# Performance work log

Hardware: AMD Instinct MI355X
Metric: run time of the kernel (lower is better)

Reference implementation:

```python
import jax, jax.numpy as jnp
import numpy as np

B, N, H, DH = 2, 512, 12, 64
DIM, DPAIR, DCOND = 768, 128, 512
INNER = 4 * DIM  # expansion_factor * dim


def _ln(x, eps=1e-5):
    m = jnp.mean(x, -1, keepdims=True)
    v = jnp.mean((x - m) ** 2, -1, keepdims=True)
    return (x - m) * jax.lax.rsqrt(v + eps)


def _rope(t):
    # t: [b,h,n,d]; standard rotary over head dim
    d = t.shape[-1]
    pos = jnp.arange(t.shape[2], dtype=t.dtype)
    inv = 1.0 / (10000.0 ** (jnp.arange(0, d, 2, dtype=t.dtype) / d))
    ang = pos[:, None] * inv[None, :]  # [n, d/2]
    cos, sin = jnp.cos(ang), jnp.sin(ang)
    t1, t2 = t[..., 0::2], t[..., 1::2]
    return jnp.stack([t1 * cos - t2 * sin, t1 * sin + t2 * cos], -1).reshape(t.shape)


def _adaln(x, cond, mask, gw, gb, bw):
    cn = _ln(cond)
    return (_ln(x) * jax.nn.sigmoid(cn @ gw + gb) + cn @ bw) * mask[..., None]


def _scale_out(x, cond, mask, w, b):
    # adaLN-zero style output scaling
    return x * jax.nn.sigmoid(_ln(cond) @ w + b) * mask[..., None]


def _windowed_attn(q, k, v, bias, pair_mask, n_queries, n_keys):
    # q/k/v: [b,h,n,d]; bias: [b,h,n,n]; pair_mask: [b,n,n]
    b, h, n, d = q.shape
    nw = n // n_queries
    centers = jnp.arange(nw) * n_queries + n_queries // 2
    idx = centers[:, None] - n_keys // 2 + jnp.arange(n_keys)[None, :]  # [nw,nk]
    valid = (idx >= 0) & (idx < n)
    idxc = jnp.clip(idx, 0, n - 1)
    qw = q.reshape(b, h, nw, n_queries, d)
    kw = k[:, :, idxc]  # [b,h,nw,nk,d]
    vw = v[:, :, idxc]
    ib = jnp.broadcast_to(idxc[None, None, :, None, :], (b, h, nw, n_queries, n_keys))
    bias_w = jnp.take_along_axis(bias.reshape(b, h, nw, n_queries, n), ib, axis=-1)
    pm = jnp.take_along_axis(
        pair_mask.reshape(b, nw, n_queries, n),
        jnp.broadcast_to(idxc[None, :, None, :], (b, nw, n_queries, n_keys)), axis=-1)
    scores = jnp.einsum('bhwqd,bhwkd->bhwqk', qw, kw) / jnp.sqrt(jnp.asarray(d, q.dtype)) + bias_w
    ok = (pm[:, None] > 0) & valid[None, None, :, None, :]
    attn = jax.nn.softmax(jnp.where(ok, scores, -1e9), axis=-1)
    out = jnp.einsum('bhwqk,bhwkd->bhwqd', attn, vw)
    return out.reshape(b, h, n, d)


def setup_inputs() -> dict:
    key = jax.random.key(0)
    ks = iter(jax.random.split(key, 48))
    nrm = lambda shape: jax.random.normal(next(ks), shape, jnp.float32) * 0.02
    return dict(
        x=jax.random.normal(next(ks), (B, N, DIM), jnp.float32),
        pair_rep=jax.random.normal(next(ks), (B, N, N, DPAIR), jnp.float32),
        cond=jax.random.normal(next(ks), (B, N, DCOND), jnp.float32),
        mask=jnp.ones((B, N), jnp.float32),
        pair_mask=jnp.ones((B, N, N), jnp.float32),
        adaln1_gw=nrm((DCOND, DIM)), adaln1_gb=jnp.zeros((DIM,), jnp.float32), adaln1_bw=nrm((DCOND, DIM)),
        wq=nrm((DIM, H * DH)), bq=jnp.zeros((H * DH,), jnp.float32),
        wk=nrm((DIM, H * DH)), bk=jnp.zeros((H * DH,), jnp.float32),
        wv=nrm((DIM, H * DH)), bv=jnp.zeros((H * DH,), jnp.float32),
        wg=nrm((DIM, H * DH)), bg=jnp.zeros((H * DH,), jnp.float32),
        wb_pair=nrm((DPAIR, H)),
        wo=nrm((H * DH, DIM)), bo=jnp.zeros((DIM,), jnp.float32),
        scale1_w=nrm((DCOND, DIM)), scale1_b=jnp.full((DIM,), -2.0, jnp.float32),
        adaln2_gw=nrm((DCOND, DIM)), adaln2_gb=jnp.zeros((DIM,), jnp.float32), adaln2_bw=nrm((DCOND, DIM)),
        tr_win=nrm((DIM, 2 * INNER)), tr_wout=nrm((INNER, DIM)),
        scale2_w=nrm((DCOND, DIM)), scale2_b=jnp.full((DIM,), -2.0, jnp.float32),
        n_queries=32, n_keys=128,
    )


def reference(x, pair_rep, cond, mask, pair_mask,
              adaln1_gw, adaln1_gb, adaln1_bw,
              wq, bq, wk, bk, wv, bv, wg, bg, wb_pair, wo, bo,
              scale1_w, scale1_b,
              adaln2_gw, adaln2_gb, adaln2_bw,
              tr_win, tr_wout,
              scale2_w, scale2_b,
              n_queries, n_keys):
    b, n, _ = x.shape
    x = x * mask[..., None]

    # --- MHA (adaLN -> pair-biased rotary windowed attention -> adaLN-zero scale) ---
    xa = _adaln(x, cond, mask, adaln1_gw, adaln1_gb, adaln1_bw)
    q = (xa @ wq + bq).reshape(b, n, H, DH).transpose(0, 2, 1, 3)
    k = (xa @ wk + bk).reshape(b, n, H, DH).transpose(0, 2, 1, 3)
    v = (xa @ wv + bv).reshape(b, n, H, DH).transpose(0, 2, 1, 3)
    q, k = _ln(q), _ln(k)      # qk layernorm
    q, k = _rope(q), _rope(k)  # rotary
    bias = jnp.einsum('bijp,ph->bhij', _ln(pair_rep), wb_pair)
    o = _windowed_attn(q, k, v, bias, pair_mask, n_queries, n_keys)
    o = o.transpose(0, 2, 1, 3).reshape(b, n, H * DH)
    attn_out = (o * jax.nn.sigmoid(xa @ wg + bg)) @ wo + bo
    attn_out = _scale_out(attn_out, cond, mask, scale1_w, scale1_b) * mask[..., None]
    x = (attn_out + x) * mask[..., None]  # residual_mha

    # --- Transition (adaLN -> SwiGLU -> adaLN-zero scale) ---
    xt = _adaln(x, cond, mask, adaln2_gw, adaln2_gb, adaln2_bw)
    a, g = jnp.split(xt @ tr_win, 2, axis=-1)
    tr = ((a * jax.nn.silu(g)) @ tr_wout) * mask[..., None]
    tr = _scale_out(tr, cond, mask, scale2_w, scale2_b) * mask[..., None]
    x = (tr + x) * mask[..., None]  # residual_transition
    return x * mask[..., None]
```

## Files before the change

### kernel.cpp

```cpp
#include <hip/hip_runtime.h>
#include <hip/hip_bf16.h>
#include <math.h>
#include <stdint.h>

#define Bc   2
#define Nc   512
#define Hc   12
#define DHc  64
#define DIMc 768
#define DPAIRc 128
#define DCONDc 512
#define INNERc 3072
#define NQc  32
#define NKc  128
#define NWc  (Nc / NQc)

typedef __attribute__((ext_vector_type(8))) short short8;
typedef __attribute__((ext_vector_type(4))) float floatx4;

__device__ inline float wave_sum(float v) {
#pragma unroll
  for (int off = 32; off > 0; off >>= 1) v += __shfl_xor(v, off, 64);
  return v;
}
__device__ inline float wave_max(float v) {
#pragma unroll
  for (int off = 32; off > 0; off >>= 1) v = fmaxf(v, __shfl_xor(v, off, 64));
  return v;
}
__device__ inline float block_sum(float v, float* red) {
  v = wave_sum(v);
  int wv = threadIdx.x >> 6, lane = threadIdx.x & 63;
  __syncthreads();
  if (lane == 0) red[wv] = v;
  __syncthreads();
  return red[0] + red[1] + red[2] + red[3];
}
__device__ inline float sigmoidf(float x) { return 1.0f / (1.0f + expf(-x)); }

__device__ __forceinline__ void gload16(const void* g, void* l) {
  __builtin_amdgcn_global_load_lds(
      reinterpret_cast<__attribute__((address_space(1))) const void*>(
          reinterpret_cast<uintptr_t>(g)),
      reinterpret_cast<__attribute__((address_space(3))) void*>(
          static_cast<uint32_t>(reinterpret_cast<uintptr_t>(l))),
      16, 0, 0);
}

__global__ __launch_bounds__(256) void ln_rows_bf16_k(const float* __restrict__ in,
                                                      __hip_bfloat16* __restrict__ out, int C) {
  __shared__ float red[4];
  int row = blockIdx.x;
  const float* x = in + (size_t)row * C;
  float s = 0.f;
  for (int c = threadIdx.x; c < C; c += 256) s += x[c];
  float mean = block_sum(s, red) / C;
  float vs = 0.f;
  for (int c = threadIdx.x; c < C; c += 256) { float d = x[c] - mean; vs += d * d; }
  float var = block_sum(vs, red) / C;
  float r = rsqrtf(var + 1e-5f);
  for (int c = threadIdx.x; c < C; c += 256)
    out[(size_t)row * C + c] = __float2bfloat16((x[c] - mean) * r);
}

struct TP6 { const float* s0; const float* s1; const float* s2;
             const float* s3; const float* s4; const float* s5; };
__global__ __launch_bounds__(256) void transpose_cast_batch_k(TP6 p,
    __hip_bfloat16* __restrict__ dstBase, int K, int N) {
  __shared__ float tile[32][33];
  const float* srcs[6] = {p.s0, p.s1, p.s2, p.s3, p.s4, p.s5};
  const float* src = srcs[blockIdx.z];
  __hip_bfloat16* dst = dstBase + (size_t)blockIdx.z * K * N;
  int k0 = blockIdx.y * 32, n0 = blockIdx.x * 32;
  int t = threadIdx.x;
  int r = t >> 5, c = t & 31;
#pragma unroll
  for (int i = 0; i < 4; ++i) tile[r + i * 8][c] = src[(size_t)(k0 + r + i * 8) * N + n0 + c];
  __syncthreads();
#pragma unroll
  for (int i = 0; i < 4; ++i)
    dst[(size_t)(n0 + r + i * 8) * K + k0 + c] = __float2bfloat16(tile[c][r + i * 8]);
}

__global__ __launch_bounds__(256) void concat_bias_k(
    const float* __restrict__ a1_gb, const float* __restrict__ s1_b,
    const float* __restrict__ a2_gb, const float* __restrict__ s2_b,
    const float* __restrict__ bq, const float* __restrict__ bk,
    const float* __restrict__ bv, const float* __restrict__ bg,
    const float* __restrict__ wb_pair,
    float* __restrict__ cb6, float* __restrict__ bqkvg,
    __hip_bfloat16* __restrict__ wbT, float* __restrict__ colsum) {
  int i = blockIdx.x * 256 + threadIdx.x;
  if (i < 6 * DIMc) {
    int seg = i / DIMc, o = i - seg * DIMc;
    float v = 0.f;
    if (seg == 0) v = a1_gb[o];
    else if (seg == 2) v = s1_b[o];
    else if (seg == 3) v = a2_gb[o];
    else if (seg == 5) v = s2_b[o];
    cb6[i] = v;
  }
  if (i < 4 * DIMc) {
    int seg = i / DIMc, o = i - seg * DIMc;
    bqkvg[i] = (seg == 0) ? bq[o] : (seg == 1) ? bk[o] : (seg == 2) ? bv[o] : bg[o];
  }
  if (i < 16 * DPAIRc) {
    int h = i >> 7, c = i & 127;
    wbT[i] = (h < Hc) ? __float2bfloat16(wb_pair[c * Hc + h]) : __float2bfloat16(0.f);
  }
  if (blockIdx.x == 0 && threadIdx.x < 16) {
    int h = threadIdx.x;
    float s = 0.f;
    if (h < Hc)
      for (int c = 0; c < DPAIRc; ++c)
        s += __bfloat162float(__float2bfloat16(wb_pair[c * Hc + h]));
    colsum[h] = s;
  }
}

template <int WNT>
__global__ __launch_bounds__(256) void gemm_bf16_k(
    const __hip_bfloat16* __restrict__ A, const __hip_bfloat16* __restrict__ Bt,
    float* __restrict__ C, int M, int N, int K,
    const float* __restrict__ bias,
    const float* __restrict__ ss, int ssst,
    const float* __restrict__ resid, const float* __restrict__ maskp, int mode) {
  constexpr int TN = 32 * WNT;
  __shared__ __align__(16) __hip_bfloat16 As[128 * 32];
  __shared__ __align__(16) __hip_bfloat16 Bs[TN * 32];
  int tid = threadIdx.x;
  int lane = tid & 63, wv = tid >> 6;
  int l16 = lane & 15, quad = lane >> 4;
  int m0 = blockIdx.y * 128, n0 = blockIdx.x * TN;
  int wm0 = (wv >> 1) * 64, wn0 = (wv & 1) * (16 * WNT);

  int srow = tid >> 2;
  int skc = (tid & 3) * 8;
  const __hip_bfloat16* Ab  = A  + (size_t)(m0 + srow) * K + skc;
  const __hip_bfloat16* Ab2 = Ab + (size_t)64 * K;
  const __hip_bfloat16* Bb  = Bt + (size_t)(n0 + srow) * K + skc;
  const __hip_bfloat16* Bb2 = Bb + (size_t)64 * K;
  __hip_bfloat16* AsW = As + wv * 512;
  __hip_bfloat16* BsW = Bs + wv * 512;

  floatx4 acc[4][WNT];
#pragma unroll
  for (int mi = 0; mi < 4; ++mi)
#pragma unroll
    for (int nj = 0; nj < WNT; ++nj) acc[mi][nj] = (floatx4){0.f, 0.f, 0.f, 0.f};

  for (int k0 = 0; k0 < K; k0 += 32) {
    gload16(Ab + k0, AsW);
    gload16(Ab2 + k0, AsW + 2048);
    if (WNT == 4) {
      gload16(Bb + k0, BsW);
      gload16(Bb2 + k0, BsW + 2048);
    } else {
      if (wv < 2) gload16(Bb + k0, BsW);
    }
    __syncthreads();
    short8 a[4], b[WNT];
#pragma unroll
    for (int mi = 0; mi < 4; ++mi)
      a[mi] = *(const short8*)(const void*)&As[(wm0 + mi * 16 + l16) * 32 + quad * 8];
#pragma unroll
    for (int nj = 0; nj < WNT; ++nj)
      b[nj] = *(const short8*)(const void*)&Bs[(wn0 + nj * 16 + l16) * 32 + quad * 8];
#pragma unroll
    for (int mi = 0; mi < 4; ++mi)
#pragma unroll
      for (int nj = 0; nj < WNT; ++nj)
        acc[mi][nj] = __builtin_amdgcn_mfma_f32_16x16x32_bf16(a[mi], b[nj], acc[mi][nj], 0, 0, 0);
    __syncthreads();
  }

#pragma unroll
  for (int mi = 0; mi < 4; ++mi) {
#pragma unroll
    for (int nj = 0; nj < WNT; ++nj) {
      int ncol = n0 + wn0 + nj * 16 + l16;
      float bb = bias ? bias[ncol] : 0.f;
#pragma unroll
      for (int r = 0; r < 4; ++r) {
        int m = m0 + wm0 + mi * 16 + quad * 4 + r;
        float v = acc[mi][nj][r] + bb;
        if (mode == 1) {
          float mk = maskp[m];
          v *= sigmoidf(ss[(size_t)m * ssst + ncol]) * mk * mk;
          v = (v + resid[(size_t)m * N + ncol]) * mk;
        } else if (mode == 2) {
          float mk = maskp[m];
          v = v * mk * sigmoidf(ss[(size_t)m * ssst + ncol]) * mk * mk;
          v = (v + resid[(size_t)m * N + ncol]) * mk * mk;
        }
        C[(size_t)m * N + ncol] = v;
      }
    }
  }
}

__global__ __launch_bounds__(256) void adaln_apply_k(
    const float* __restrict__ xin, const float* __restrict__ maskp,
    const float* __restrict__ graw, const float* __restrict__ braw, int ssst,
    __hip_bfloat16* __restrict__ xa, float* __restrict__ xm) {
  __shared__ float red[4];
  int row = blockIdx.x;
  float mk = maskp[row];
  const float* xr = xin + (size_t)row * DIMc;
  float vals[3];
  float s = 0.f;
#pragma unroll
  for (int it = 0; it < 3; ++it) {
    int c = threadIdx.x + it * 256;
    float v = xr[c] * mk;
    vals[it] = v;
    s += v;
  }
  float mean = block_sum(s, red) * (1.0f / DIMc);
  float vs = 0.f;
#pragma unroll
  for (int it = 0; it < 3; ++it) { float d = vals[it] - mean; vs += d * d; }
  float var = block_sum(vs, red) * (1.0f / DIMc);
  float r = rsqrtf(var + 1e-5f);
#pragma unroll
  for (int it = 0; it < 3; ++it) {
    int c = threadIdx.x + it * 256;
    size_t sidx = (size_t)row * ssst + c;
    if (xm) xm[(size_t)row * DIMc + c] = vals[it];
    float o = ((vals[it] - mean) * r * sigmoidf(graw[sidx]) + braw[sidx]) * mk;
    xa[(size_t)row * DIMc + c] = __float2bfloat16(o);
  }
}

__global__ __launch_bounds__(256) void lnrope_k(float* __restrict__ qkvg) {
  float* q = qkvg + blockIdx.y * DIMc;
  int rowid = blockIdx.x * 4 + (threadIdx.x >> 6);
  int lane = threadIdx.x & 63;
  int bn = rowid / Hc;
  int h = rowid - bn * Hc;
  int n = bn & (Nc - 1);
  size_t base = (size_t)bn * (4 * DIMc) + h * DHc;
  float v = q[base + lane];
  float mean = wave_sum(v) * (1.0f / 64.0f);
  float d = v - mean;
  float var = wave_sum(d * d) * (1.0f / 64.0f);
  float vn = d * rsqrtf(var + 1e-5f);
  int i = lane >> 1;
  float inv = exp2f(-(float)i * 0.415241011861f);
  float ang = (float)n * inv;
  float c = cosf(ang), s = sinf(ang);
  float partner = __shfl_xor(vn, 1, 64);
  float out = (lane & 1) ? (partner * s + vn * c) : (vn * c - partner * s);
  q[base + lane] = out;
}

__global__ __launch_bounds__(256) void pair_bias_mfma_k(
    const float* __restrict__ pr, const __hip_bfloat16* __restrict__ wbT,
    const float* __restrict__ colsum, float* __restrict__ biasw) {
  constexpr int LDR = 136;
  __shared__ __hip_bfloat16 rows[128 * LDR];
  __shared__ float meanS[128];
  __shared__ float rstdS[128];
  int bi = blockIdx.x;
  int i = bi & (Nc - 1), b = bi >> 9;
  int w = i >> 5, qi = i & 31;
  int j0 = w * NQc - 48;
  int t = threadIdx.x;
  int sub = t >> 5;
  int c4 = t & 31;
  const float* prb = pr + (size_t)bi * (Nc * DPAIRc);
#pragma unroll
  for (int step = 0; step < 16; ++step) {
    int row = step * 8 + sub;
    int jc = min(max(j0 + row, 0), Nc - 1);
    float4 v = *(const float4*)(prb + (size_t)jc * DPAIRc + c4 * 4);
    union { __hip_bfloat16 h[4]; uint2 u; } pk;
    pk.h[0] = __float2bfloat16(v.x); pk.h[1] = __float2bfloat16(v.y);
    pk.h[2] = __float2bfloat16(v.z); pk.h[3] = __float2bfloat16(v.w);
    *(uint2*)(void*)&rows[row * LDR + c4 * 4] = pk.u;
    float s = v.x + v.y + v.z + v.w;
    float s2 = v.x * v.x + v.y * v.y + v.z * v.z + v.w * v.w;
#pragma unroll
    for (int off = 16; off > 0; off >>= 1) {
      s += __shfl_xor(s, off, 64);
      s2 += __shfl_xor(s2, off, 64);
    }
    if (c4 == 0) {
      float mean = s * (1.0f / 128.0f);
      float var = s2 * (1.0f / 128.0f) - mean * mean;
      meanS[row] = mean;
      rstdS[row] = rsqrtf(var + 1e-5f);
    }
  }
  __syncthreads();
  int lane = t & 63, wv = t >> 6;
  int l16 = lane & 15, quad = lane >> 4;
  short8 bfrag[4];
#pragma unroll
  for (int ks = 0; ks < 4; ++ks)
    bfrag[ks] = *(const short8*)(const void*)&wbT[l16 * 128 + ks * 32 + quad * 8];
  float cs = colsum[l16];
#pragma unroll
  for (int mt = 0; mt < 2; ++mt) {
    int mtile = wv * 2 + mt;
    floatx4 acc = (floatx4){0.f, 0.f, 0.f, 0.f};
#pragma unroll
    for (int ks = 0; ks < 4; ++ks) {
      short8 a = *(const short8*)(const void*)&rows[(mtile * 16 + l16) * LDR + ks * 32 + quad * 8];
      acc = __builtin_amdgcn_mfma_f32_16x16x32_bf16(a, bfrag[ks], acc, 0, 0, 0);
    }
    if (l16 < Hc) {
      int m0r = mtile * 16 + quad * 4;
      float4 ov;
      float* po = &ov.x;
#pragma unroll
      for (int r = 0; r < 4; ++r) {
        int m = m0r + r;
        po[r] = rstdS[m] * (acc[r] - meanS[m] * cs);
      }
      *(float4*)&biasw[((((size_t)(b * Hc + l16)) * NWc + w) * NQc + qi) * NKc + m0r] = ov;
    }
  }
}

__global__ __launch_bounds__(256) void wattn_k(
    const float* __restrict__ qkvg, const float* __restrict__ biasw,
    const float* __restrict__ pair_mask, __hip_bfloat16* __restrict__ o) {
  constexpr int LQ = 72;
  constexpr int LV = 136;
  constexpr int LS = 132;
  constexpr int LP = 136;
  __shared__ __hip_bfloat16 qs[32 * LQ];
  __shared__ __hip_bfloat16 ks[128 * LQ];
  __shared__ __hip_bfloat16 vT[64 * LV];
  __shared__ float sc[32 * LS];
  __shared__ __hip_bfloat16 scP[32 * LP];
  const int QS = 4 * DIMc;
  int blk = blockIdx.x;
  int w = blk & (NWc - 1);
  int bh = blk >> 4;
  int h = bh % Hc;
  int b = bh / Hc;
  int t = threadIdx.x;
  int j0 = w * NQc - 48;
  for (int e = t; e < 512; e += 256) {
    int qrow = e >> 4, c4 = e & 15;
    float4 v = *(const float4*)&qkvg[(size_t)(b * Nc + w * NQc + qrow) * QS + h * DHc + c4 * 4];
    union { __hip_bfloat16 hh[4]; uint2 u; } pk;
    pk.hh[0] = __float2bfloat16(v.x); pk.hh[1] = __float2bfloat16(v.y);
    pk.hh[2] = __float2bfloat16(v.z); pk.hh[3] = __float2bfloat16(v.w);
    *(uint2*)(void*)&qs[qrow * LQ + c4 * 4] = pk.u;
  }
  for (int e = t; e < 2048; e += 256) {
    int kk = e >> 4, c4 = e & 15;
    int jc = min(max(j0 + kk, 0), Nc - 1);
    size_t src = (size_t)(b * Nc + jc) * QS + h * DHc + c4 * 4;
    float4 kv = *(const float4*)&qkvg[src + DIMc];
    float4 vv = *(const float4*)&qkvg[src + 2 * DIMc];
    union { __hip_bfloat16 hh[4]; uint2 u; } pk;
    pk.hh[0] = __float2bfloat16(kv.x); pk.hh[1] = __float2bfloat16(kv.y);
    pk.hh[2] = __float2bfloat16(kv.z); pk.hh[3] = __float2bfloat16(kv.w);
    *(uint2*)(void*)&ks[kk * LQ + c4 * 4] = pk.u;
    vT[(c4 * 4 + 0) * LV + kk] = __float2bfloat16(vv.x);
    vT[(c4 * 4 + 1) * LV + kk] = __float2bfloat16(vv.y);
    vT[(c4 * 4 + 2) * LV + kk] = __float2bfloat16(vv.z);
    vT[(c4 * 4 + 3) * LV + kk] = __float2bfloat16(vv.w);
  }
  for (int e = t; e < 4096; e += 256) {
    int qrow = e >> 7, key = e & 127;
    int j = j0 + key;
    bool valid = (j >= 0) && (j < Nc);
    int jc = min(max(j, 0), Nc - 1);
    float pm = pair_mask[((size_t)(b * Nc + w * NQc + qrow)) * Nc + jc];
    bool ok = valid && (pm > 0.f);
    sc[qrow * LS + key] = ok ? biasw[((size_t)blk * 32 + qrow) * 128 + key] : -1e30f;
  }
  __syncthreads();
  int lane = t & 63, wv = t >> 6;
  int l16 = lane & 15, quad = lane >> 4;
  {
    short8 bfr[2][2];
#pragma unroll
    for (int nt = 0; nt < 2; ++nt)
#pragma unroll
      for (int k2 = 0; k2 < 2; ++k2)
        bfr[nt][k2] = *(const short8*)(const void*)&ks[(wv * 32 + nt * 16 + l16) * LQ + k2 * 32 + quad * 8];
#pragma unroll
    for (int mi = 0; mi < 2; ++mi) {
      short8 afr[2];
#pragma unroll
      for (int k2 = 0; k2 < 2; ++k2)
        afr[k2] = *(const short8*)(const void*)&qs[(mi * 16 + l16) * LQ + k2 * 32 + quad * 8];
#pragma unroll
      for (int nt = 0; nt < 2; ++nt) {
        floatx4 acc = (floatx4){0.f, 0.f, 0.f, 0.f};
        acc = __builtin_amdgcn_mfma_f32_16x16x32_bf16(afr[0], bfr[nt][0], acc, 0, 0, 0);
        acc = __builtin_amdgcn_mfma_f32_16x16x32_bf16(afr[1], bfr[nt][1], acc, 0, 0, 0);
        int key = wv * 32 + nt * 16 + l16;
#pragma unroll
        for (int r = 0; r < 4; ++r) {
          int m = mi * 16 + quad * 4 + r;
          float sv = sc[m * LS + key];
          if (sv > -1e29f) sc[m * LS + key] = sv + acc[r] * 0.125f;
        }
      }
    }
  }
  __syncthreads();
#pragma unroll
  for (int rr = 0; rr < 8; ++rr) {
    int qq = wv * 8 + rr;
    float v0 = sc[qq * LS + lane], v1 = sc[qq * LS + 64 + lane];
    float mx = wave_max(fmaxf(v0, v1));
    float e0 = expf(v0 - mx), e1 = expf(v1 - mx);
    float inv = 1.0f / wave_sum(e0 + e1);
    scP[qq * LP + lane] = __float2bfloat16(e0 * inv);
    scP[qq * LP + 64 + lane] = __float2bfloat16(e1 * inv);
  }
  __syncthreads();
  {
    short8 vb[4];
#pragma unroll
    for (int k4 = 0; k4 < 4; ++k4)
      vb[k4] = *(const short8*)(const void*)&vT[(wv * 16 + l16) * LV + k4 * 32 + quad * 8];
#pragma unroll
    for (int mi = 0; mi < 2; ++mi) {
      floatx4 acc = (floatx4){0.f, 0.f, 0.f, 0.f};
#pragma unroll
      for (int k4 = 0; k4 < 4; ++k4) {
        short8 pa = *(const short8*)(const void*)&scP[(mi * 16 + l16) * LP + k4 * 32 + quad * 8];
        acc = __builtin_amdgcn_mfma_f32_16x16x32_bf16(pa, vb[k4], acc, 0, 0, 0);
      }
      int d = wv * 16 + l16;
#pragma unroll
      for (int r = 0; r < 4; ++r) {
        int m = mi * 16 + quad * 4 + r;
        size_t mrow = (size_t)(b * Nc + w * NQc + m);
        float g = qkvg[mrow * QS + 3 * DIMc + h * DHc + d];
        o[mrow * DIMc + h * DHc + d] = __float2bfloat16(acc[r] * sigmoidf(g));
      }
    }
  }
}

__global__ __launch_bounds__(256) void silu_gate_k(const float* __restrict__ h,
                                                   __hip_bfloat16* __restrict__ act, int total) {
  int i = blockIdx.x * 256 + threadIdx.x;
  if (i < total) {
    int m = i / INNERc, j = i - m * INNERc;
    float a = h[(size_t)m * (2 * INNERc) + j];
    float g = h[(size_t)m * (2 * INNERc) + INNERc + j];
    act[i] = __float2bfloat16(a * g * sigmoidf(g));
  }
}

extern "C" void kernel_launch(void* const* d_in, const int* in_sizes, int n_in,
                              void* d_out, int out_size, void* d_ws, size_t ws_size,
                              hipStream_t stream) {
  const float* x        = (const float*)d_in[0];
  const float* pair_rep = (const float*)d_in[1];
  const float* cond     = (const float*)d_in[2];
  const float* mask     = (const float*)d_in[3];
  const float* pair_mask= (const float*)d_in[4];
  const float* a1_gw    = (const float*)d_in[5];
  const float* a1_gb    = (const float*)d_in[6];
  const float* a1_bw    = (const float*)d_in[7];
  const float* wq       = (const float*)d_in[8];
  const float* bq       = (const float*)d_in[9];
  const float* wk       = (const float*)d_in[10];
  const float* bk       = (const float*)d_in[11];
  const float* wv       = (const float*)d_in[12];
  const float* bv       = (const float*)d_in[13];
  const float* wg       = (const float*)d_in[14];
  const float* bg       = (const float*)d_in[15];
  const float* wb_pair  = (const float*)d_in[16];
  const float* wo       = (const float*)d_in[17];
  const float* bo       = (const float*)d_in[18];
  const float* s1_w     = (const float*)d_in[19];
  const float* s1_b     = (const float*)d_in[20];
  const float* a2_gw    = (const float*)d_in[21];
  const float* a2_gb    = (const float*)d_in[22];
  const float* a2_bw    = (const float*)d_in[23];
  const float* tr_win   = (const float*)d_in[24];
  const float* tr_wout  = (const float*)d_in[25];
  const float* s2_w     = (const float*)d_in[26];
  const float* s2_b     = (const float*)d_in[27];
  float* out = (float*)d_out;

  const int M = Bc * Nc;
  char* wsb = (char*)d_ws;
  size_t off = 0;
  auto alloc = [&](size_t bytes) { void* p = wsb + off; off += (bytes + 255) & ~(size_t)255; return p; };

  __hip_bfloat16* cnb     = (__hip_bfloat16*)alloc((size_t)M * DCONDc * 2);
  __hip_bfloat16* Wc6t    = (__hip_bfloat16*)alloc((size_t)6 * DIMc * DCONDc * 2);
  __hip_bfloat16* Wqkvg5t = (__hip_bfloat16*)alloc((size_t)5 * DIMc * DIMc * 2);
  __hip_bfloat16* twint   = (__hip_bfloat16*)alloc((size_t)2 * INNERc * DIMc * 2);
  __hip_bfloat16* twoutt  = (__hip_bfloat16*)alloc((size_t)DIMc * INNERc * 2);
  float* cb6    = (float*)alloc((size_t)6 * DIMc * 4);
  float* bqkvg  = (float*)alloc((size_t)4 * DIMc * 4);
  __hip_bfloat16* wbT = (__hip_bfloat16*)alloc((size_t)16 * DPAIRc * 2);
  float* colsum = (float*)alloc(16 * 4);
  float* proj_c = (float*)alloc((size_t)M * 6 * DIMc * 4);
  float* xm     = (float*)alloc((size_t)M * DIMc * 4);
  __hip_bfloat16* xa = (__hip_bfloat16*)alloc((size_t)M * DIMc * 2);
  float* qkvg   = (float*)alloc((size_t)M * 4 * DIMc * 4);
  float* biasw  = (float*)alloc((size_t)Bc * Hc * NWc * NQc * NKc * 4);
  __hip_bfloat16* obg = (__hip_bfloat16*)alloc((size_t)M * DIMc * 2);
  float* x2     = (float*)alloc((size_t)M * DIMc * 4);
  __hip_bfloat16* xt = (__hip_bfloat16*)alloc((size_t)M * DIMc * 2);
  float* hb     = (float*)alloc((size_t)M * 2 * INNERc * 4);
  __hip_bfloat16* actb = (__hip_bfloat16*)alloc((size_t)M * INNERc * 2);
  __hip_bfloat16* wot = Wqkvg5t + (size_t)4 * DIMc * DIMc;
  (void)ws_size; (void)in_sizes; (void)n_in; (void)out_size;

  dim3 blk(256);

  ln_rows_bf16_k<<<M, blk, 0, stream>>>(cond, cnb, DCONDc);

  transpose_cast_batch_k<<<dim3(DIMc / 32, DCONDc / 32, 6), blk, 0, stream>>>(
      TP6{a1_gw, a1_bw, s1_w, a2_gw, a2_bw, s2_w}, Wc6t, DCONDc, DIMc);
  transpose_cast_batch_k<<<dim3(DIMc / 32, DIMc / 32, 5), blk, 0, stream>>>(
      TP6{wq, wk, wv, wg, wo, wo}, Wqkvg5t, DIMc, DIMc);
  transpose_cast_batch_k<<<dim3(2 * INNERc / 32, DIMc / 32, 1), blk, 0, stream>>>(
      TP6{tr_win, tr_win, tr_win, tr_win, tr_win, tr_win}, twint, DIMc, 2 * INNERc);
  transpose_cast_batch_k<<<dim3(DIMc / 32, INNERc / 32, 1), blk, 0, stream>>>(
      TP6{tr_wout, tr_wout, tr_wout, tr_wout, tr_wout, tr_wout}, twoutt, INNERc, DIMc);

  concat_bias_k<<<(6 * DIMc + 255) / 256, blk, 0, stream>>>(
      a1_gb, s1_b, a2_gb, s2_b, bq, bk, bv, bg, wb_pair, cb6, bqkvg, wbT, colsum);

  gemm_bf16_k<4><<<dim3(6 * DIMc / 128, M / 128), blk, 0, stream>>>(
      cnb, Wc6t, proj_c, M, 6 * DIMc, DCONDc, cb6, nullptr, 0, nullptr, nullptr, 0);

  adaln_apply_k<<<M, blk, 0, stream>>>(x, mask, proj_c + 0, proj_c + DIMc, 6 * DIMc, xa, xm);

  gemm_bf16_k<4><<<dim3(4 * DIMc / 128, M / 128), blk, 0, stream>>>(
      xa, Wqkvg5t, qkvg, M, 4 * DIMc, DIMc, bqkvg, nullptr, 0, nullptr, nullptr, 0);

  lnrope_k<<<dim3((M * Hc) / 4, 2), blk, 0, stream>>>(qkvg);

  pair_bias_mfma_k<<<Bc * Nc, blk, 0, stream>>>(pair_rep, wbT, colsum, biasw);

  wattn_k<<<Bc * Hc * NWc, blk, 0, stream>>>(qkvg, biasw, pair_mask, obg);

  gemm_bf16_k<1><<<dim3(DIMc / 32, M / 128), blk, 0, stream>>>(
      obg, wot, x2, M, DIMc, DIMc, bo, proj_c + 2 * DIMc, 6 * DIMc, xm, mask, 1);

  adaln_apply_k<<<M, blk, 0, stream>>>(x2, mask, proj_c + 3 * DIMc, proj_c + 4 * DIMc,
                                       6 * DIMc, xt, nullptr);

  gemm_bf16_k<4><<<dim3(2 * INNERc / 128, M / 128), blk, 0, stream>>>(
      xt, twint, hb, M, 2 * INNERc, DIMc, nullptr, nullptr, 0, nullptr, nullptr, 0);

  silu_gate_k<<<(M * INNERc + 255) / 256, blk, 0, stream>>>(hb, actb, M * INNERc);

  gemm_bf16_k<1><<<dim3(DIMc / 32, M / 128), blk, 0, stream>>>(
      actb, twoutt, out, M, DIMc, INNERc, nullptr, proj_c + 5 * DIMc, 6 * DIMc, x2, mask, 2);
}
```

Before: 616.2 us.

## Double-buffer LDS tiles in bf16 GEMM to overlap loads with MFMA

```diff
diff --git a/kernel.cpp b/kernel.cpp
--- a/kernel.cpp
+++ b/kernel.cpp
@@ -126,8 +126,8 @@
     const float* __restrict__ ss, int ssst,
     const float* __restrict__ resid, const float* __restrict__ maskp, int mode) {
   constexpr int TN = 32 * WNT;
-  __shared__ __align__(16) __hip_bfloat16 As[128 * 32];
-  __shared__ __align__(16) __hip_bfloat16 Bs[TN * 32];
+  __shared__ __align__(16) __hip_bfloat16 As[2][128 * 32];
+  __shared__ __align__(16) __hip_bfloat16 Bs[2][TN * 32];
   int tid = threadIdx.x;
   int lane = tid & 63, wv = tid >> 6;
   int l16 = lane & 15, quad = lane >> 4;
@@ -140,8 +140,10 @@
   const __hip_bfloat16* Ab2 = Ab + (size_t)64 * K;
   const __hip_bfloat16* Bb  = Bt + (size_t)(n0 + srow) * K + skc;
   const __hip_bfloat16* Bb2 = Bb + (size_t)64 * K;
-  __hip_bfloat16* AsW = As + wv * 512;
-  __hip_bfloat16* BsW = Bs + wv * 512;
+  __hip_bfloat16* AsW0 = &As[0][0] + wv * 512;
+  __hip_bfloat16* AsW1 = &As[1][0] + wv * 512;
+  __hip_bfloat16* BsW0 = &Bs[0][0] + wv * 512;
+  __hip_bfloat16* BsW1 = &Bs[1][0] + wv * 512;
 
   floatx4 acc[4][WNT];
 #pragma unroll
@@ -149,28 +151,39 @@
 #pragma unroll
     for (int nj = 0; nj < WNT; ++nj) acc[mi][nj] = (floatx4){0.f, 0.f, 0.f, 0.f};
 
-  for (int k0 = 0; k0 < K; k0 += 32) {
-    gload16(Ab + k0, AsW);
-    gload16(Ab2 + k0, AsW + 2048);
+  auto stage = [&](int kk, __hip_bfloat16* AW, __hip_bfloat16* BW) {
+    gload16(Ab + kk, AW);
+    gload16(Ab2 + kk, AW + 2048);
     if (WNT == 4) {
-      gload16(Bb + k0, BsW);
-      gload16(Bb2 + k0, BsW + 2048);
+      gload16(Bb + kk, BW);
+      gload16(Bb2 + kk, BW + 2048);
     } else {
-      if (wv < 2) gload16(Bb + k0, BsW);
-    }
-    __syncthreads();
+      if (wv < 2) gload16(Bb + kk, BW);
+    }
+  };
+  auto compute = [&](const __hip_bfloat16* Asb, const __hip_bfloat16* Bsb) {
     short8 a[4], b[WNT];
 #pragma unroll
     for (int mi = 0; mi < 4; ++mi)
-      a[mi] = *(const short8*)(const void*)&As[(wm0 + mi * 16 + l16) * 32 + quad * 8];
+      a[mi] = *(const short8*)(const void*)&Asb[(wm0 + mi * 16 + l16) * 32 + quad * 8];
 #pragma unroll
     for (int nj = 0; nj < WNT; ++nj)
-      b[nj] = *(const short8*)(const void*)&Bs[(wn0 + nj * 16 + l16) * 32 + quad * 8];
+      b[nj] = *(const short8*)(const void*)&Bsb[(wn0 + nj * 16 + l16) * 32 + quad * 8];
 #pragma unroll
     for (int mi = 0; mi < 4; ++mi)
 #pragma unroll
       for (int nj = 0; nj < WNT; ++nj)
         acc[mi][nj] = __builtin_amdgcn_mfma_f32_16x16x32_bf16(a[mi], b[nj], acc[mi][nj], 0, 0, 0);
+  };
+
+  stage(0, AsW0, BsW0);
+  __syncthreads();
+  for (int k0 = 0; k0 < K; k0 += 64) {
+    if (k0 + 32 < K) stage(k0 + 32, AsW1, BsW1);
+    compute(&As[0][0], &Bs[0][0]);
+    __syncthreads();
+    if (k0 + 64 < K) stage(k0 + 64, AsW0, BsW0);
+    compute(&As[1][0], &Bs[1][0]);
     __syncthreads();
   }
 
```

Result: faster. 592.8 us (-3.8%).
